# Performance work log

Measured on AMD Instinct MI355X. Metric: run time of the kernel, lower is better.

The kernel has to match this reference:

```python
import jax, jax.numpy as jnp
import numpy as np
import math

B, S, D, H = 2, 4096, 768, 12
HD = D // H            # 64
BLK = 32               # MRA block size (hard-coded in the module)
NBR = S // BLK         # 128 blocks per row
NUM_BLOCK = 1024       # selected score blocks per (batch*head)
APPROX_MODE = "full"
FIRST_N = 0            # initial_prior_first_n_blocks
DIAG_N = 3             # initial_prior_diagonal_n_blocks
MB = B * H


def setup_inputs() -> dict:
    key = jax.random.key(0)
    ks = jax.random.split(key, 4)
    scale = 0.02
    return {
        "X": jax.random.normal(ks[0], (B, S, D), jnp.float32),
        "mask": jnp.ones((B, S), jnp.float32),
        "Wq": scale * jax.random.normal(ks[1], (D, D), jnp.float32),
        "bq": jnp.zeros((D,), jnp.float32),
        "Wk": scale * jax.random.normal(ks[2], (D, D), jnp.float32),
        "bk": jnp.zeros((D,), jnp.float32),
        "Wv": scale * jax.random.normal(ks[3], (D, D), jnp.float32),
        "bv": jnp.zeros((D,), jnp.float32),
    }


def _mra2_attention(Q, K, V, mask):
    # Q, K, V: [MB, S, HD]; mask: [MB, S] (float 0/1)
    inv_sqrt_d = 1.0 / math.sqrt(HD)
    Q = Q * mask[:, :, None]
    K = K * mask[:, :, None]
    V = V * mask[:, :, None]

    # ---- low-resolution (block-mean) logits ----
    token_count = mask.reshape(MB, NBR, BLK).sum(-1)                 # [MB, NBR]
    denom = token_count[:, :, None] + 1e-6
    Qh = Q.reshape(MB, NBR, BLK, HD).sum(2) / denom                  # [MB, NBR, HD]
    Kh = K.reshape(MB, NBR, BLK, HD).sum(2) / denom
    Vh = V.reshape(MB, NBR, BLK, HD).sum(2) / denom

    low_logit = jnp.einsum('bnd,bmd->bnm', Qh, Kh) * inv_sqrt_d      # [MB, NBR, NBR]
    row_max = low_logit.max(-1, keepdims=True)                        # [MB, NBR, 1] (before empty-pair masking)
    pair_empty = (token_count[:, None, :] * token_count[:, :, None]) < 0.5
    low_logit = low_logit - 1e4 * pair_empty.astype(low_logit.dtype)

    # ---- top-k block selection (no grad) ----
    prior = jax.lax.stop_gradient(low_logit - row_max)
    if DIAG_N > 0:
        off = DIAG_N // 2
        i = jnp.arange(NBR)
        band = (jnp.abs(i[:, None] - i[None, :]) <= off).astype(prior.dtype)
        prior = prior + band[None] * 5e3
    if FIRST_N > 0:
        prior = prior.at[:, :FIRST_N, :].add(5e3)
        prior = prior.at[:, :, :FIRST_N].add(5e3)
    top_vals, indices = jax.lax.top_k(prior.reshape(MB, -1), NUM_BLOCK)  # row-major flat idx = q_blk*NBR + k_blk
    threshold = top_vals.min(-1)
    selected_mask = (prior >= threshold[:, None, None]).astype(jnp.float32)  # 1 for selected low-res blocks

    rblk = indices // NBR   # query block index, [MB, NUM_BLOCK]
    cblk = indices % NBR    # key block index
    bidx = jnp.arange(MB)[:, None]

    Qb = Q.reshape(MB, NBR, BLK, HD)
    Kb = K.reshape(MB, NBR, BLK, HD)
    Vb = V.reshape(MB, NBR, BLK, HD)
    kmask = mask.reshape(MB, NBR, BLK)[bidx, cblk]                   # [MB, NB, 32k]

    Qg = Qb[bidx, rblk]                                              # [MB, NB, 32, HD]
    Kg = Kb[bidx, cblk]
    Vg = Vb[bidx, cblk]

    # ---- high-resolution sparse block logits ----
    logit = jnp.einsum('bnqd,bnkd->bnqk', Qg, Kg) * inv_sqrt_d       # [MB, NB, 32q, 32k]

    seg = (jnp.arange(MB)[:, None] * NBR + rblk).reshape(-1)         # segment id per block -> query row block
    blk_qmax = logit.max(-1).reshape(MB * NUM_BLOCK, BLK)            # per-query-token max within block
    max_rows = jax.ops.segment_max(blk_qmax, seg, num_segments=MB * NBR)
    max_rows = jnp.maximum(max_rows, -1e6).reshape(MB, NBR, BLK)     # guard rows w/o selected blocks
    max_vals = max_rows.reshape(MB, S)                               # per-token sparse row max
    max_scatter = max_rows[bidx, rblk]                               # [MB, NB, 32q]

    logit = logit - max_scatter[:, :, :, None]
    logit = logit - 1e4 * (1.0 - kmask[:, :, None, :])
    attn = jnp.exp(logit)

    blk_out = jnp.einsum('bnqk,bnkd->bnqd', attn, Vg)                # [MB, NB, 32, HD]
    high_out = jax.ops.segment_sum(
        blk_out.reshape(MB * NUM_BLOCK, BLK, HD), seg, num_segments=MB * NBR
    ).reshape(MB, S, HD)
    high_norm = jax.ops.segment_sum(
        attn.sum(-1).reshape(MB * NUM_BLOCK, BLK), seg, num_segments=MB * NBR
    ).reshape(MB, S)

    if APPROX_MODE == "full":
        # low-res attention over NON-selected blocks, weighted by token counts
        low_attn = jnp.exp(low_logit - row_max - 1e4 * selected_mask) * token_count[:, None, :]
        low_out = jnp.einsum('bnm,bmd->bnd', low_attn, Vh)           # [MB, NBR, HD]
        low_out = jnp.repeat(low_out[:, :, None, :], BLK, axis=2).reshape(MB, S, HD)
        low_norm = jnp.repeat(low_attn.sum(-1)[:, :, None], BLK, axis=2).reshape(MB, S)

        log_corr = jnp.repeat(row_max, BLK, axis=2).reshape(MB, S) - max_vals
        log_corr = log_corr * mask
        low_corr = jnp.exp(jnp.minimum(log_corr, 0.0))
        high_corr = jnp.exp(-jnp.maximum(log_corr, 0.0))

        out = (high_out * high_corr[:, :, None] + low_out * low_corr[:, :, None]) / (
            (high_norm * high_corr + low_norm * low_corr + 1e-6)[:, :, None]
        )
    else:  # "sparse"
        out = high_out / (high_norm[:, :, None] + 1e-6)
    return out


def reference(X, mask, Wq, bq, Wk, bk, Wv, bv):
    def proj(W, b):
        y = jnp.einsum('bsd,ed->bse', X, W) + b                       # nn.Linear: x @ W.T + b
        return y.reshape(B, S, H, HD).transpose(0, 2, 1, 3).reshape(MB, S, HD)

    Q, K, V = proj(Wq, bq), proj(Wk, bk), proj(Wv, bv)
    m = jnp.broadcast_to(mask[:, None, :], (B, H, S)).reshape(MB, S)
    out = _mra2_attention(Q, K, V, m)
    return out.reshape(B, H, S, HD).transpose(0, 2, 1, 3).reshape(B, S, D)
```

## Files before the change

### kernel.cpp

```cpp
#include <hip/hip_runtime.h>

typedef __bf16 bf16;
typedef float f32x4 __attribute__((ext_vector_type(4)));
typedef bf16 bf16x8 __attribute__((ext_vector_type(8)));
typedef bf16 bf16x4 __attribute__((ext_vector_type(4)));
typedef unsigned int uint;
typedef unsigned short ushort;


__device__ __forceinline__ void llds16(const bf16* g, bf16* l) {
    __builtin_amdgcn_global_load_lds((const __attribute__((address_space(1))) uint*)g,
                                     (__attribute__((address_space(3))) uint*)l, 16, 0, 0);
}

__device__ __forceinline__ uint sortable(float f) {
    uint u = __float_as_uint(f);
    return u ^ (uint)(((int)u >> 31) | 0x80000000);
}

__global__ __launch_bounds__(256)
void k_prep(const float* __restrict__ X, const float* __restrict__ mask,
            bf16* __restrict__ Xb, float* __restrict__ Xh, float* __restrict__ tc) {
    const int row = blockIdx.x;
    const int b = row >> 7, nbr = row & 127;
    const int g = blockIdx.y;
    const int t = threadIdx.x;
    const int c = t & 63;
    const int tq = t >> 6;
    const int c4 = g * 64 + c;
    const size_t base = (size_t)(b * 4096 + nbr * 32) * 768;
    const float4* xp = (const float4*)(X + base) + c4;
    bf16x4* xbp = (bf16x4*)(Xb + base) + c4;
    const float* mp = mask + b * 4096 + nbr * 32;
    __shared__ float4 red[4][64];
    __shared__ float tcr[4];
    float4 s = {0.f, 0.f, 0.f, 0.f};
    float tcs = 0.f;
#pragma unroll
    for (int j = 0; j < 8; ++j) {
        const int tok = tq * 8 + j;
        float4 v = xp[(size_t)tok * 192];
        float m = mp[tok];
        s.x += v.x * m; s.y += v.y * m; s.z += v.z * m; s.w += v.w * m;
        tcs += m;
        bf16x4 o = {(bf16)v.x, (bf16)v.y, (bf16)v.z, (bf16)v.w};
        xbp[(size_t)tok * 192] = o;
    }
    red[tq][c] = s;
    if (c == 0) tcr[tq] = tcs;
    __syncthreads();
    if (tq == 0) {
        float4 a = red[0][c], b2 = red[1][c], c2 = red[2][c], d2 = red[3][c];
        float4 o = {a.x + b2.x + c2.x + d2.x, a.y + b2.y + c2.y + d2.y,
                    a.z + b2.z + c2.z + d2.z, a.w + b2.w + c2.w + d2.w};
        ((float4*)(Xh + (size_t)row * 768))[c4] = o;
        if (c == 0 && g == 0) tc[row] = tcr[0] + tcr[1] + tcr[2] + tcr[3];
    }
}

__global__ void k_convW(const float* __restrict__ Wq, const float* __restrict__ Wk,
                        const float* __restrict__ Wv, bf16* __restrict__ Wb) {
    int i = blockIdx.x * 256 + threadIdx.x;
    if (i >= 442368) return;
    int n = (i << 2) / 768;
    int k = (i << 2) % 768;
    const float* W = n < 768 ? Wq : (n < 1536 ? Wk : Wv);
    int nn = n - (n < 768 ? 0 : (n < 1536 ? 768 : 1536));
    float4 f = *(const float4*)(W + (size_t)nn * 768 + k);
    bf16x4 o = {(bf16)f.x, (bf16)f.y, (bf16)f.z, (bf16)f.w};
    ((bf16x4*)Wb)[i] = o;
}

__global__ __launch_bounds__(256, 4)
void k_gemm_qkv(const bf16* __restrict__ Xb, const bf16* __restrict__ Wb,
                const float* __restrict__ bq, const float* __restrict__ bk,
                const float* __restrict__ bv, const float* __restrict__ mask,
                bf16* __restrict__ Qb, bf16* __restrict__ Kb, bf16* __restrict__ Vt) {
    __shared__ bf16 smem[17408];
    bf16* As = smem;
    bf16* Bs = smem + 8192;
    const int tid = threadIdx.x;
    const int wave = tid >> 6, lane = tid & 63;
    const int quad = lane >> 4, l16 = lane & 15;
    const int wr = wave >> 1, wc = wave & 1;
    const int m0 = blockIdx.x * 128, n0 = blockIdx.y * 128;
    const int srow = lane >> 3;
    const int sgcol = (((lane & 7) ^ (srow & 7)) << 3);

    f32x4 acc[4][4] = {};

    for (int k0 = 0; k0 < 768; k0 += 64) {
        __syncthreads();
#pragma unroll
        for (int it = 0; it < 4; ++it) {
            int R = wave * 32 + it * 8;
            llds16(Xb + (size_t)(m0 + R + srow) * 768 + k0 + sgcol, &As[R * 64]);
            llds16(Wb + (size_t)(n0 + R + srow) * 768 + k0 + sgcol, &Bs[R * 64]);
        }
        __syncthreads();
#pragma unroll
        for (int ks = 0; ks < 2; ++ks) {
            const int pg = ((ks * 4 + quad) ^ (l16 & 7)) << 3;
            bf16x8 a[4], b[4];
#pragma unroll
            for (int i = 0; i < 4; ++i)
                a[i] = *(const bf16x8*)&As[(wr * 64 + i * 16 + l16) * 64 + pg];
#pragma unroll
            for (int i = 0; i < 4; ++i)
                b[i] = *(const bf16x8*)&Bs[(wc * 64 + i * 16 + l16) * 64 + pg];
#pragma unroll
            for (int i = 0; i < 4; ++i)
#pragma unroll
                for (int j = 0; j < 4; ++j)
                    acc[i][j] = __builtin_amdgcn_mfma_f32_16x16x32_bf16(a[i], b[j], acc[i][j], 0, 0, 0);
        }
    }

    const int which = n0 / 768;
    const float* bias = which == 0 ? bq : (which == 1 ? bk : bv);

    __syncthreads();
#pragma unroll
    for (int i = 0; i < 4; ++i) {
        const int rloc0 = wr * 64 + i * 16 + quad * 4;
#pragma unroll
        for (int j = 0; j < 4; ++j) {
            const int cloc = wc * 64 + j * 16 + l16;
            const int hcol = n0 - which * 768 + cloc;
            const float bv_ = bias[hcol];
#pragma unroll
            for (int r = 0; r < 4; ++r) {
                const int rloc = rloc0 + r;
                const int mm = m0 + rloc;
                const int bidx = mm >> 12, s = mm & 4095;
                const float y = (acc[i][j][r] + bv_) * mask[(bidx << 12) + s];
                if (which == 2) smem[cloc * 136 + rloc] = (bf16)y;
                else            smem[rloc * 136 + cloc] = (bf16)y;
            }
        }
    }
    __syncthreads();
    if (which < 2) {
        bf16* dst = which == 0 ? Qb : Kb;
#pragma unroll
        for (int it = 0; it < 8; ++it) {
            const int gidx = it * 256 + tid;
            const int sr = gidx >> 4, chunk = gidx & 15;
            const int mm = m0 + sr;
            const int bidx = mm >> 12, s = mm & 4095;
            const int hcol = n0 - which * 768 + chunk * 8;
            const int h = hcol >> 6, d0 = hcol & 63;
            bf16x8 v = *(const bf16x8*)&smem[sr * 136 + chunk * 8];
            *(bf16x8*)(dst + ((((size_t)(bidx * 12 + h)) << 12) + s) * 64 + d0) = v;
        }
    } else {
#pragma unroll
        for (int it = 0; it < 8; ++it) {
            const int gidx = it * 256 + tid;
            const int drow = gidx >> 4, chunk = gidx & 15;
            const int s0 = chunk * 8;
            const int mm = m0 + s0;
            const int bidx = mm >> 12, s = mm & 4095;
            const int hcol = n0 - 1536 + drow;
            const int h = hcol >> 6, dd = hcol & 63;
            bf16x8 v = *(const bf16x8*)&smem[drow * 136 + s0];
            *(bf16x8*)(Vt + ((((size_t)(bidx * 12 + h)) * 128 + (s >> 5)) * 64 + dd) * 32 + (s & 31)) = v;
        }
    }
}

__global__ __launch_bounds__(256)
void k_lowres_p(const float* __restrict__ Xh,
                const float* __restrict__ Wq, const float* __restrict__ Wk,
                const float* __restrict__ Wv, float* __restrict__ partial) {
    const int nb = blockIdx.x;
    const int rowbase = blockIdx.y * 128;
    const int bz = blockIdx.z;
    const int kb = bz * 112;
    const int klen = (bz == 6) ? 96 : 112;
    const int t = threadIdx.x;

    __shared__ float As[16 * 132];
    __shared__ float Bs[16 * 132];

    const int which = nb / 6;
    const float* Wsel = which == 0 ? Wq : (which == 1 ? Wk : Wv);
    const float* Wbase = Wsel + (size_t)((nb % 6) * 128) * 768;

    const int sr = t >> 2;
    const int skq = t & 3;
    const int tr = t >> 4, tc2 = t & 15;
    const int r0 = tr * 8, c0 = tc2 * 8;

    float acc[8][8] = {};
    float4 va[2], vb[2];
    const int stages = klen >> 4;

#pragma unroll
    for (int i = 0; i < 2; ++i) {
        va[i] = *(const float4*)(Xh + (size_t)(rowbase + sr + 64 * i) * 768 + kb + skq * 4);
        vb[i] = *(const float4*)(Wbase + (size_t)(sr + 64 * i) * 768 + kb + skq * 4);
    }

    for (int s = 0; s < stages; ++s) {
        __syncthreads();
#pragma unroll
        for (int i = 0; i < 2; ++i) {
            const int r = sr + 64 * i;
            As[(skq * 4 + 0) * 132 + r] = va[i].x;
            As[(skq * 4 + 1) * 132 + r] = va[i].y;
            As[(skq * 4 + 2) * 132 + r] = va[i].z;
            As[(skq * 4 + 3) * 132 + r] = va[i].w;
            Bs[(skq * 4 + 0) * 132 + r] = vb[i].x;
            Bs[(skq * 4 + 1) * 132 + r] = vb[i].y;
            Bs[(skq * 4 + 2) * 132 + r] = vb[i].z;
            Bs[(skq * 4 + 3) * 132 + r] = vb[i].w;
        }
        if (s + 1 < stages) {
            const int kc = kb + (s + 1) * 16;
#pragma unroll
            for (int i = 0; i < 2; ++i) {
                va[i] = *(const float4*)(Xh + (size_t)(rowbase + sr + 64 * i) * 768 + kc + skq * 4);
                vb[i] = *(const float4*)(Wbase + (size_t)(sr + 64 * i) * 768 + kc + skq * 4);
            }
        }
        __syncthreads();
#pragma unroll
        for (int k = 0; k < 16; ++k) {
            float4 a0 = *(const float4*)&As[k * 132 + r0];
            float4 a1 = *(const float4*)&As[k * 132 + r0 + 4];
            float4 b0 = *(const float4*)&Bs[k * 132 + c0];
            float4 b1 = *(const float4*)&Bs[k * 132 + c0 + 4];
            float av[8] = {a0.x, a0.y, a0.z, a0.w, a1.x, a1.y, a1.z, a1.w};
            float bv[8] = {b0.x, b0.y, b0.z, b0.w, b1.x, b1.y, b1.z, b1.w};
#pragma unroll
            for (int i = 0; i < 8; ++i)
#pragma unroll
                for (int j = 0; j < 8; ++j)
                    acc[i][j] += av[i] * bv[j];
        }
    }

    float* pp = partial + (size_t)bz * 589824 + (size_t)(rowbase + r0) * 2304 + nb * 128 + c0;
#pragma unroll
    for (int i = 0; i < 8; ++i) {
        float4 s0 = {acc[i][0], acc[i][1], acc[i][2], acc[i][3]};
        float4 s1 = {acc[i][4], acc[i][5], acc[i][6], acc[i][7]};
        *(float4*)(pp + (size_t)i * 2304) = s0;
        *(float4*)(pp + (size_t)i * 2304 + 4) = s1;
    }
}

__global__ __launch_bounds__(256)
void k_lowfin(const float* __restrict__ partial, const float* __restrict__ tc,
              const float* __restrict__ bq, const float* __restrict__ bk,
              const float* __restrict__ bv,
              float* __restrict__ Qh, float* __restrict__ Kh, float* __restrict__ Vh) {
    const int gx = blockIdx.x;
    const int row = blockIdx.y;
    const int t = threadIdx.x;
    const int gcol = gx * 256 + t;
    float s = 0.f;
#pragma unroll
    for (int ch = 0; ch < 7; ++ch)
        s += partial[(size_t)ch * 589824 + (size_t)row * 2304 + gcol];
    const int which = gx / 3;
    const int wcol = (gx % 3) * 256 + t;
    const float* bias = which == 0 ? bq : (which == 1 ? bk : bv);
    const float tcv = tc[row];
    const float val = (s + tcv * bias[wcol]) / (tcv + 1e-6f);
    const int b = row >> 7, nbr = row & 127;
    const int h = wcol >> 6, d = wcol & 63;
    float* dst = which == 0 ? Qh : (which == 1 ? Kh : Vh);
    dst[(((size_t)(b * 12 + h)) * 128 + nbr) * 64 + d] = val;
}

__global__ __launch_bounds__(256)
void k_lowlogit(const float* __restrict__ Qh, const float* __restrict__ Kh,
                float* __restrict__ prior, float* __restrict__ rowmax) {
    int mb = blockIdx.x, rc = blockIdx.y;
    int tid = threadIdx.x;
    __shared__ float Ksh[64 * 132];
    __shared__ float Qsh[16 * 64];
    for (int idx = tid; idx < 128 * 64; idx += 256) {
        int c = idx >> 6, k = idx & 63;
        Ksh[k * 132 + c] = Kh[((size_t)mb * 128 + c) * 64 + k];
    }
    for (int idx = tid; idx < 16 * 64; idx += 256) {
        int r = idx >> 6, k = idx & 63;
        Qsh[idx] = Qh[((size_t)mb * 128 + rc * 16 + r) * 64 + k];
    }
    __syncthreads();
    int rloc = tid >> 4, cg = tid & 15;
    float acc[8] = {};
    for (int k = 0; k < 64; ++k) {
        float qv = Qsh[rloc * 64 + k];
        const float* kr = &Ksh[k * 132 + cg * 8];
#pragma unroll
        for (int j = 0; j < 8; ++j) acc[j] += qv * kr[j];
    }
    float pm = -3.4e38f;
#pragma unroll
    for (int j = 0; j < 8; ++j) { acc[j] *= 0.125f; pm = fmaxf(pm, acc[j]); }
#pragma unroll
    for (int d = 1; d < 16; d <<= 1) pm = fmaxf(pm, __shfl_xor(pm, d, 64));
    int r = rc * 16 + rloc;
    if (cg == 0) rowmax[mb * 128 + r] = pm;
    float* dst = prior + ((size_t)mb * 128 + r) * 128 + cg * 8;
#pragma unroll
    for (int j = 0; j < 8; ++j) dst[j] = acc[j] - pm;
}

__global__ __launch_bounds__(1024)
void k_select(const float* __restrict__ prior, unsigned char* __restrict__ selmask,
              unsigned short* __restrict__ lists, int* __restrict__ counts,
              ushort* __restrict__ qorder) {
    const int mb = blockIdx.x, tid = threadIdx.x;
    const int ln = tid & 63;
    __shared__ int lc[16 * 3];
    __shared__ int cnt[128];
    if (tid < 48) lc[tid] = 0;
    if (tid < 128) cnt[tid] = 0;

    const int r = tid >> 3;
    const int cbase = (tid & 7) << 4;
    uint key[16];
    const float4* P4 = (const float4*)(prior + (size_t)mb * 16384) + (tid << 2);
#pragma unroll
    for (int j4 = 0; j4 < 4; ++j4) {
        float4 v = P4[j4];
        float vv[4] = {v.x, v.y, v.z, v.w};
#pragma unroll
        for (int e = 0; e < 4; ++e) {
            int c = cbase + (j4 << 2) + e;
            float f = vv[e] + ((r - c <= 1 && c - r <= 1) ? 5e3f : 0.f);
            key[(j4 << 2) + e] = sortable(f);
        }
    }
    __syncthreads();

    uint pfx = 0u;
    int k = 1024;
#pragma unroll
    for (int lvl = 0; lvl < 16; ++lvl) {
        const int sh = 30 - 2 * lvl;
        const uint maskA = (lvl == 0) ? 0u : (0xFFFFFFFFu << (sh + 2));
        int c3 = 0, c2 = 0, c1 = 0;
#pragma unroll
        for (int j = 0; j < 16; ++j) {
            uint x = key[j];
            bool m = ((x ^ pfx) & maskA) == 0u;
            uint f = (x >> sh) & 3u;
            c3 += (m && f == 3u);
            c2 += (m && f == 2u);
            c1 += (m && f == 1u);
        }
#pragma unroll
        for (int d = 1; d < 64; d <<= 1) {
            c3 += __shfl_xor(c3, d, 64);
            c2 += __shfl_xor(c2, d, 64);
            c1 += __shfl_xor(c1, d, 64);
        }
        if (ln == 0) {
            atomicAdd(&lc[lvl * 3 + 0], c3);
            atomicAdd(&lc[lvl * 3 + 1], c2);
            atomicAdd(&lc[lvl * 3 + 2], c1);
        }
        __syncthreads();
        const int C3 = lc[lvl * 3 + 0], C2 = lc[lvl * 3 + 1], C1 = lc[lvl * 3 + 2];
        uint choose;
        if (C3 >= k)                { choose = 3u; }
        else if (C3 + C2 >= k)      { choose = 2u; k -= C3; }
        else if (C3 + C2 + C1 >= k) { choose = 1u; k -= C3 + C2; }
        else                        { choose = 0u; k -= C3 + C2 + C1; }
        pfx |= choose << sh;
    }
    const uint T = pfx;

    uint packed[4] = {0u, 0u, 0u, 0u};
#pragma unroll
    for (int j = 0; j < 16; ++j) {
        if (key[j] >= T) {
            packed[j >> 2] |= 1u << ((j & 3) << 3);
            int pos = atomicAdd(&cnt[r], 1);
            lists[((size_t)mb * 128 + r) * 128 + pos] = (unsigned short)(cbase + j);
        }
    }
    uint4 pk;
    pk.x = packed[0]; pk.y = packed[1]; pk.z = packed[2]; pk.w = packed[3];
    *(uint4*)(selmask + (size_t)mb * 16384 + (size_t)tid * 16) = pk;
    __syncthreads();
    if (tid < 128) {
        const int myc = cnt[tid];
        counts[mb * 128 + tid] = myc;
        int rank = 0;
        for (int j = 0; j < 128; ++j) {
            int cj = cnt[j];
            rank += (cj > myc) || (cj == myc && j < tid);
        }
        qorder[mb * 128 + rank] = (ushort)tid;
    }
}

__global__ __launch_bounds__(64)
void k_lowout(const float* __restrict__ prior, const unsigned char* __restrict__ selmask,
              const float* __restrict__ tc, const float* __restrict__ Vh,
              float* __restrict__ low_out, float* __restrict__ low_norm) {
    const int q = blockIdx.x & 127, mb = blockIdx.x >> 7;
    const int d = threadIdx.x;
    const float* pn = prior + ((size_t)mb * 128 + q) * 128;
    const uint4* smv = (const uint4*)(selmask + ((size_t)mb * 128 + q) * 128);
    uint sm32[32];
#pragma unroll
    for (int w = 0; w < 8; ++w) {
        uint4 u = smv[w];
        sm32[w * 4 + 0] = u.x; sm32[w * 4 + 1] = u.y;
        sm32[w * 4 + 2] = u.z; sm32[w * 4 + 3] = u.w;
    }
    const float* tcb = tc + (mb / 12) * 128;
    const float* Vb = Vh + (size_t)mb * 128 * 64;
    float acc = 0.f, nrm = 0.f;
#pragma unroll 4
    for (int c = 0; c < 128; ++c) {
        if (!((sm32[c >> 2] >> ((c & 3) << 3)) & 1u)) {
            float w = __expf(pn[c]) * tcb[c];
            acc += w * Vb[c * 64 + d];
            nrm += w;
        }
    }
    low_out[((size_t)mb * 128 + q) * 64 + d] = acc;
    if (d == 0) low_norm[mb * 128 + q] = nrm;
}

__global__ __launch_bounds__(64)
void k_high(const bf16* __restrict__ Qb, const bf16* __restrict__ Kb,
            const bf16* __restrict__ Vt, const int* __restrict__ counts,
            const unsigned short* __restrict__ lists, const ushort* __restrict__ qorder,
            const float* __restrict__ rowmax, const float* __restrict__ low_out,
            const float* __restrict__ low_norm, const float* __restrict__ mask,
            float* __restrict__ out) {
    const int bid = blockIdx.x;
    const int work = ((bid & 7) * 384) + (bid >> 3);
    const int mb = work >> 7;
    const int q = qorder[mb * 128 + (work & 127)];
    const int lane = threadIdx.x, quad = lane >> 4, l16 = lane & 15;
    __shared__ bf16 Pa[32 * 40];
    __shared__ bf16 Pbs[32 * 40];

    const bf16* Qbase = Qb + ((size_t)mb * 4096 + q * 32) * 64;
    bf16x8 qf[2][2];
#pragma unroll
    for (int mt = 0; mt < 2; ++mt)
#pragma unroll
        for (int ks = 0; ks < 2; ++ks)
            qf[mt][ks] = *(const bf16x8*)(Qbase + (mt * 16 + l16) * 64 + ks * 32 + quad * 8);

    bf16x8 ones;
#pragma unroll
    for (int j = 0; j < 8; ++j) ones[j] = (bf16)1.0f;

    float mxl[2][4];
    f32x4 o[2][4] = {};
    f32x4 lac[2] = {};
#pragma unroll
    for (int mt = 0; mt < 2; ++mt)
#pragma unroll
        for (int r = 0; r < 4; ++r) mxl[mt][r] = -3.4e38f;

    int cntv = counts[mb * 128 + q];
    if (cntv > 128) cntv = 128;
    if (cntv < 1) cntv = 1;
    const uint* lst32 = (const uint*)(lists + ((size_t)mb * 128 + q) * 128);

    const bf16* KB = Kb + (size_t)mb * 4096 * 64;
    const bf16* VB = Vt + (size_t)mb * 128 * 2048;

    int koff[2][2], voff[4];
#pragma unroll
    for (int nt = 0; nt < 2; ++nt)
#pragma unroll
        for (int ks = 0; ks < 2; ++ks) koff[nt][ks] = (nt * 16 + l16) * 64 + ks * 32 + quad * 8;
#pragma unroll
    for (int nd = 0; nd < 4; ++nd) voff[nd] = (nd * 16 + l16) * 32 + quad * 8;

    bf16x8 kA[2][2], vA[4], kB[2][2], vB[4];
    {
        const uint pr = lst32[0];
        const int cA = __builtin_amdgcn_readfirstlane((int)(pr & 0xffffu));
        const bf16* kp = KB + (size_t)cA * 2048;
        const bf16* vp = VB + (size_t)cA * 2048;
#pragma unroll
        for (int nt = 0; nt < 2; ++nt)
#pragma unroll
            for (int ks = 0; ks < 2; ++ks) kA[nt][ks] = *(const bf16x8*)(kp + koff[nt][ks]);
#pragma unroll
        for (int nd = 0; nd < 4; ++nd) vA[nd] = *(const bf16x8*)(vp + voff[nd]);
        if (cntv > 1) {
            const int cB = __builtin_amdgcn_readfirstlane((int)(pr >> 16));
            const bf16* kp2 = KB + (size_t)cB * 2048;
            const bf16* vp2 = VB + (size_t)cB * 2048;
#pragma unroll
            for (int nt = 0; nt < 2; ++nt)
#pragma unroll
                for (int ks = 0; ks < 2; ++ks) kB[nt][ks] = *(const bf16x8*)(kp2 + koff[nt][ks]);
#pragma unroll
            for (int nd = 0; nd < 4; ++nd) vB[nd] = *(const bf16x8*)(vp2 + voff[nd]);
        }
    }

    for (int i = 0; i < cntv; i += 2) {
        const bool hasB = (i + 1 < cntv);
        const bool hasAn = (i + 2 < cntv);
        const bool hasBn = (i + 3 < cntv);
        int cAn = 0, cBn = 0;
        if (hasAn) {
            const uint prn = lst32[(i >> 1) + 1];
            cAn = __builtin_amdgcn_readfirstlane((int)(prn & 0xffffu));
            cBn = __builtin_amdgcn_readfirstlane((int)(prn >> 16));
        }

        {
            f32x4 sf[2][2] = {};
            __builtin_amdgcn_s_setprio(1);
#pragma unroll
            for (int mt = 0; mt < 2; ++mt)
#pragma unroll
                for (int nt = 0; nt < 2; ++nt) {
                    sf[mt][nt] = __builtin_amdgcn_mfma_f32_16x16x32_bf16(qf[mt][0], kA[nt][0], sf[mt][nt], 0, 0, 0);
                    sf[mt][nt] = __builtin_amdgcn_mfma_f32_16x16x32_bf16(qf[mt][1], kA[nt][1], sf[mt][nt], 0, 0, 0);
                }
            __builtin_amdgcn_s_setprio(0);
#pragma unroll
            for (int mt = 0; mt < 2; ++mt)
#pragma unroll
                for (int r = 0; r < 4; ++r) {
                    mxl[mt][r] = fmaxf(mxl[mt][r], fmaxf(sf[mt][0][r], sf[mt][1][r]));
                    float e0, e1;
                    asm("v_exp_f32 %0, %1" : "=v"(e0) : "v"(sf[mt][0][r] * 0.18033688011112042f));
                    asm("v_exp_f32 %0, %1" : "=v"(e1) : "v"(sf[mt][1][r] * 0.18033688011112042f));
                    Pa[(mt * 16 + quad * 4 + r) * 40 + l16] = (bf16)e0;
                    Pa[(mt * 16 + quad * 4 + r) * 40 + 16 + l16] = (bf16)e1;
                }
        }
        if (hasB) {
            f32x4 sf[2][2] = {};
            __builtin_amdgcn_s_setprio(1);
#pragma unroll
            for (int mt = 0; mt < 2; ++mt)
#pragma unroll
                for (int nt = 0; nt < 2; ++nt) {
                    sf[mt][nt] = __builtin_amdgcn_mfma_f32_16x16x32_bf16(qf[mt][0], kB[nt][0], sf[mt][nt], 0, 0, 0);
                    sf[mt][nt] = __builtin_amdgcn_mfma_f32_16x16x32_bf16(qf[mt][1], kB[nt][1], sf[mt][nt], 0, 0, 0);
                }
            __builtin_amdgcn_s_setprio(0);
#pragma unroll
            for (int mt = 0; mt < 2; ++mt)
#pragma unroll
                for (int r = 0; r < 4; ++r) {
                    mxl[mt][r] = fmaxf(mxl[mt][r], fmaxf(sf[mt][0][r], sf[mt][1][r]));
                    float e0, e1;
                    asm("v_exp_f32 %0, %1" : "=v"(e0) : "v"(sf[mt][0][r] * 0.18033688011112042f));
                    asm("v_exp_f32 %0, %1" : "=v"(e1) : "v"(sf[mt][1][r] * 0.18033688011112042f));
                    Pbs[(mt * 16 + quad * 4 + r) * 40 + l16] = (bf16)e0;
                    Pbs[(mt * 16 + quad * 4 + r) * 40 + 16 + l16] = (bf16)e1;
                }
        }

        if (hasAn) {
            const bf16* kp = KB + (size_t)cAn * 2048;
#pragma unroll
            for (int nt = 0; nt < 2; ++nt)
#pragma unroll
                for (int ks = 0; ks < 2; ++ks) kA[nt][ks] = *(const bf16x8*)(kp + koff[nt][ks]);
        }
        if (hasBn) {
            const bf16* kp = KB + (size_t)cBn * 2048;
#pragma unroll
            for (int nt = 0; nt < 2; ++nt)
#pragma unroll
                for (int ks = 0; ks < 2; ++ks) kB[nt][ks] = *(const bf16x8*)(kp + koff[nt][ks]);
        }

        asm volatile("s_waitcnt lgkmcnt(0)" ::: "memory");
        bf16x8 pa[2], pb[2];
#pragma unroll
        for (int mt = 0; mt < 2; ++mt)
            pa[mt] = *(const bf16x8*)&Pa[(mt * 16 + l16) * 40 + quad * 8];
        if (hasB) {
#pragma unroll
            for (int mt = 0; mt < 2; ++mt)
                pb[mt] = *(const bf16x8*)&Pbs[(mt * 16 + l16) * 40 + quad * 8];
        }
        __builtin_amdgcn_s_setprio(1);
#pragma unroll
        for (int mt = 0; mt < 2; ++mt) {
#pragma unroll
            for (int nd = 0; nd < 4; ++nd)
                o[mt][nd] = __builtin_amdgcn_mfma_f32_16x16x32_bf16(pa[mt], vA[nd], o[mt][nd], 0, 0, 0);
            lac[mt] = __builtin_amdgcn_mfma_f32_16x16x32_bf16(pa[mt], ones, lac[mt], 0, 0, 0);
        }
        if (hasB) {
#pragma unroll
            for (int mt = 0; mt < 2; ++mt) {
#pragma unroll
                for (int nd = 0; nd < 4; ++nd)
                    o[mt][nd] = __builtin_amdgcn_mfma_f32_16x16x32_bf16(pb[mt], vB[nd], o[mt][nd], 0, 0, 0);
                lac[mt] = __builtin_amdgcn_mfma_f32_16x16x32_bf16(pb[mt], ones, lac[mt], 0, 0, 0);
            }
        }
        __builtin_amdgcn_s_setprio(0);

        if (hasAn) {
            const bf16* vp = VB + (size_t)cAn * 2048;
#pragma unroll
            for (int nd = 0; nd < 4; ++nd) vA[nd] = *(const bf16x8*)(vp + voff[nd]);
        }
        if (hasBn) {
            const bf16* vp = VB + (size_t)cBn * 2048;
#pragma unroll
            for (int nd = 0; nd < 4; ++nd) vB[nd] = *(const bf16x8*)(vp + voff[nd]);
        }
    }

#pragma unroll
    for (int d = 1; d < 16; d <<= 1)
#pragma unroll
        for (int mt = 0; mt < 2; ++mt)
#pragma unroll
            for (int r = 0; r < 4; ++r)
                mxl[mt][r] = fmaxf(mxl[mt][r], __shfl_xor(mxl[mt][r], d, 64));

    const int b = mb / 12, h = mb - b * 12;
    const float rm = rowmax[mb * 128 + q];
    const float ln = low_norm[mb * 128 + q];
    const float* LO = low_out + ((size_t)mb * 128 + q) * 64;
#pragma unroll
    for (int mt = 0; mt < 2; ++mt)
#pragma unroll
        for (int r = 0; r < 4; ++r) {
            const int s = q * 32 + mt * 16 + quad * 4 + r;
            const float mv = fmaxf(mxl[mt][r] * 0.125f, -1e6f);
            const float hn = lac[mt][r];
            const float mk = mask[(b << 12) + s];
            const float lcr = (rm - mv) * mk;
            const float lcf = __expf(fminf(lcr, 0.f));
            const float hcf = __expf(-mv - fmaxf(lcr, 0.f));
            const float den = 1.0f / (hn * hcf + ln * lcf + 1e-6f);
            float* op = out + ((size_t)(b * 4096 + s)) * 768 + h * 64;
#pragma unroll
            for (int nd = 0; nd < 4; ++nd) {
                const int d = nd * 16 + l16;
                op[d] = (o[mt][nd][r] * hcf + LO[d] * lcf) * den;
            }
        }
}

extern "C" void kernel_launch(void* const* d_in, const int* in_sizes, int n_in,
                              void* d_out, int out_size, void* d_ws, size_t ws_size,
                              hipStream_t stream) {
    (void)in_sizes; (void)n_in; (void)out_size; (void)ws_size;
    const float* X    = (const float*)d_in[0];
    const float* mask = (const float*)d_in[1];
    const float* Wq   = (const float*)d_in[2];
    const float* bq   = (const float*)d_in[3];
    const float* Wk   = (const float*)d_in[4];
    const float* bk   = (const float*)d_in[5];
    const float* Wv   = (const float*)d_in[6];
    const float* bv   = (const float*)d_in[7];
    float* out = (float*)d_out;

    char* ws = (char*)d_ws;
    size_t off = 0;
    auto alloc = [&](size_t bytes) -> void* {
        off = (off + 255) & ~(size_t)255;
        void* p = ws + off;
        off += bytes;
        return p;
    };
    bf16* Xb  = (bf16*)alloc((size_t)8192 * 768 * 2);
    bf16* Wb  = (bf16*)alloc((size_t)2304 * 768 * 2);
    bf16* Qb  = (bf16*)alloc((size_t)24 * 4096 * 64 * 2);
    bf16* Kb  = (bf16*)alloc((size_t)24 * 4096 * 64 * 2);
    bf16* Vt  = (bf16*)alloc((size_t)24 * 4096 * 64 * 2);
    float* Xh = (float*)alloc((size_t)256 * 768 * 4);
    float* tc = (float*)alloc(256 * 4);
    float* Qh = (float*)alloc((size_t)24 * 128 * 64 * 4);
    float* Kh = (float*)alloc((size_t)24 * 128 * 64 * 4);
    float* Vh = (float*)alloc((size_t)24 * 128 * 64 * 4);
    float* prior = (float*)alloc((size_t)24 * 16384 * 4);
    float* rowmax = (float*)alloc(24 * 128 * 4);
    unsigned char* selmask = (unsigned char*)alloc((size_t)24 * 16384);
    unsigned short* lists = (unsigned short*)alloc((size_t)24 * 128 * 128 * 2);
    int* counts = (int*)alloc(24 * 128 * 4);
    ushort* qorder = (ushort*)alloc(24 * 128 * 2);
    float* low_out   = (float*)alloc((size_t)24 * 128 * 64 * 4);
    float* low_norm  = (float*)alloc(24 * 128 * 4);
    float* partial   = (float*)alloc((size_t)7 * 589824 * 4);

    k_prep<<<dim3(256, 3), 256, 0, stream>>>(X, mask, Xb, Xh, tc);
    k_convW<<<1728, 256, 0, stream>>>(Wq, Wk, Wv, Wb);
    k_gemm_qkv<<<dim3(64, 18), 256, 0, stream>>>(Xb, Wb, bq, bk, bv, mask, Qb, Kb, Vt);
    k_lowres_p<<<dim3(18, 2, 7), 256, 0, stream>>>(Xh, Wq, Wk, Wv, partial);
    k_lowfin<<<dim3(9, 256), 256, 0, stream>>>(partial, tc, bq, bk, bv, Qh, Kh, Vh);
    k_lowlogit<<<dim3(24, 8), 256, 0, stream>>>(Qh, Kh, prior, rowmax);
    k_select<<<24, 1024, 0, stream>>>(prior, selmask, lists, counts, qorder);
    k_lowout<<<3072, 64, 0, stream>>>(prior, selmask, tc, Vh, low_out, low_norm);
    k_high<<<3072, 64, 0, stream>>>(Qb, Kb, Vt, counts, lists, qorder, rowmax, low_out,
                                    low_norm, mask, out);
}
```

Before: 268.3 us.

## Fuse weight conversion into prep and low-res output into high-res kernel

Merges the weight bf16 conversion kernel into the prep kernel as extra blocks, and computes the low-resolution attention output per query block inside k_high, after the first K/V prefetch is issued, instead of in a separate k_lowout kernel. This removes two kernel launches and the low_out/low_norm round-trip through global memory, and lets the low-res loop overlap with outstanding K/V loads. In exchange, k_high does more scalar work per block and holds more registers, and the low-res value is redistributed across lanes with shuffles during the output store.

Result: faster. 260.4 us (-2.9%).

```diff
diff --git a/kernel.cpp b/kernel.cpp
--- a/kernel.cpp
+++ b/kernel.cpp
@@ -20,11 +20,27 @@
 
 __global__ __launch_bounds__(256)
 void k_prep(const float* __restrict__ X, const float* __restrict__ mask,
-            bf16* __restrict__ Xb, float* __restrict__ Xh, float* __restrict__ tc) {
-    const int row = blockIdx.x;
+            const float* __restrict__ Wq, const float* __restrict__ Wk,
+            const float* __restrict__ Wv,
+            bf16* __restrict__ Xb, float* __restrict__ Xh, float* __restrict__ tc,
+            bf16* __restrict__ Wb) {
+    const int p = blockIdx.x;
+    const int t = threadIdx.x;
+    if (p >= 768) {
+        int i = (p - 768) * 256 + t;
+        if (i >= 442368) return;
+        int n = (i << 2) / 768;
+        int k = (i << 2) % 768;
+        const float* W = n < 768 ? Wq : (n < 1536 ? Wk : Wv);
+        int nn = n - (n < 768 ? 0 : (n < 1536 ? 768 : 1536));
+        float4 f = *(const float4*)(W + (size_t)nn * 768 + k);
+        bf16x4 o = {(bf16)f.x, (bf16)f.y, (bf16)f.z, (bf16)f.w};
+        ((bf16x4*)Wb)[i] = o;
+        return;
+    }
+    const int row = p % 256;
+    const int g = p / 256;
     const int b = row >> 7, nbr = row & 127;
-    const int g = blockIdx.y;
-    const int t = threadIdx.x;
     const int c = t & 63;
     const int tq = t >> 6;
     const int c4 = g * 64 + c;
@@ -56,19 +72,6 @@
         ((float4*)(Xh + (size_t)row * 768))[c4] = o;
         if (c == 0 && g == 0) tc[row] = tcr[0] + tcr[1] + tcr[2] + tcr[3];
     }
-}
-
-__global__ void k_convW(const float* __restrict__ Wq, const float* __restrict__ Wk,
-                        const float* __restrict__ Wv, bf16* __restrict__ Wb) {
-    int i = blockIdx.x * 256 + threadIdx.x;
-    if (i >= 442368) return;
-    int n = (i << 2) / 768;
-    int k = (i << 2) % 768;
-    const float* W = n < 768 ? Wq : (n < 1536 ? Wk : Wv);
-    int nn = n - (n < 768 ? 0 : (n < 1536 ? 768 : 1536));
-    float4 f = *(const float4*)(W + (size_t)nn * 768 + k);
-    bf16x4 o = {(bf16)f.x, (bf16)f.y, (bf16)f.z, (bf16)f.w};
-    ((bf16x4*)Wb)[i] = o;
 }
 
 __global__ __launch_bounds__(256, 4)
@@ -403,41 +406,12 @@
 }
 
 __global__ __launch_bounds__(64)
-void k_lowout(const float* __restrict__ prior, const unsigned char* __restrict__ selmask,
-              const float* __restrict__ tc, const float* __restrict__ Vh,
-              float* __restrict__ low_out, float* __restrict__ low_norm) {
-    const int q = blockIdx.x & 127, mb = blockIdx.x >> 7;
-    const int d = threadIdx.x;
-    const float* pn = prior + ((size_t)mb * 128 + q) * 128;
-    const uint4* smv = (const uint4*)(selmask + ((size_t)mb * 128 + q) * 128);
-    uint sm32[32];
-#pragma unroll
-    for (int w = 0; w < 8; ++w) {
-        uint4 u = smv[w];
-        sm32[w * 4 + 0] = u.x; sm32[w * 4 + 1] = u.y;
-        sm32[w * 4 + 2] = u.z; sm32[w * 4 + 3] = u.w;
-    }
-    const float* tcb = tc + (mb / 12) * 128;
-    const float* Vb = Vh + (size_t)mb * 128 * 64;
-    float acc = 0.f, nrm = 0.f;
-#pragma unroll 4
-    for (int c = 0; c < 128; ++c) {
-        if (!((sm32[c >> 2] >> ((c & 3) << 3)) & 1u)) {
-            float w = __expf(pn[c]) * tcb[c];
-            acc += w * Vb[c * 64 + d];
-            nrm += w;
-        }
-    }
-    low_out[((size_t)mb * 128 + q) * 64 + d] = acc;
-    if (d == 0) low_norm[mb * 128 + q] = nrm;
-}
-
-__global__ __launch_bounds__(64)
 void k_high(const bf16* __restrict__ Qb, const bf16* __restrict__ Kb,
             const bf16* __restrict__ Vt, const int* __restrict__ counts,
             const unsigned short* __restrict__ lists, const ushort* __restrict__ qorder,
-            const float* __restrict__ rowmax, const float* __restrict__ low_out,
-            const float* __restrict__ low_norm, const float* __restrict__ mask,
+            const float* __restrict__ rowmax, const float* __restrict__ prior,
+            const unsigned char* __restrict__ selmask, const float* __restrict__ tc,
+            const float* __restrict__ Vh, const float* __restrict__ mask,
             float* __restrict__ out) {
     const int bid = blockIdx.x;
     const int work = ((bid & 7) * 384) + (bid >> 3);
@@ -505,6 +479,22 @@
                 for (int ks = 0; ks < 2; ++ks) kB[nt][ks] = *(const bf16x8*)(kp2 + koff[nt][ks]);
 #pragma unroll
             for (int nd = 0; nd < 4; ++nd) vB[nd] = *(const bf16x8*)(vp2 + voff[nd]);
+        }
+    }
+
+    float lo = 0.f, ln = 0.f;
+    {
+        const float* pn = prior + ((size_t)mb * 128 + q) * 128;
+        const uint* sel32 = (const uint*)(selmask + ((size_t)mb * 128 + q) * 128);
+        const float* tcb = tc + (mb / 12) * 128;
+        const float* Vb = Vh + (size_t)mb * 128 * 64;
+#pragma unroll 4
+        for (int c = 0; c < 128; ++c) {
+            if (!((sel32[c >> 2] >> ((c & 3) << 3)) & 1u)) {
+                float w = __expf(pn[c]) * tcb[c];
+                lo += w * Vb[c * 64 + lane];
+                ln += w;
+            }
         }
     }
 
@@ -632,8 +622,6 @@
 
     const int b = mb / 12, h = mb - b * 12;
     const float rm = rowmax[mb * 128 + q];
-    const float ln = low_norm[mb * 128 + q];
-    const float* LO = low_out + ((size_t)mb * 128 + q) * 64;
 #pragma unroll
     for (int mt = 0; mt < 2; ++mt)
 #pragma unroll
@@ -650,7 +638,8 @@
 #pragma unroll
             for (int nd = 0; nd < 4; ++nd) {
                 const int d = nd * 16 + l16;
-                op[d] = (o[mt][nd][r] * hcf + LO[d] * lcf) * den;
+                const float LOd = __shfl(lo, d, 64);
+                op[d] = (o[mt][nd][r] * hcf + LOd * lcf) * den;
             }
         }
 }
@@ -693,18 +682,14 @@
     unsigned short* lists = (unsigned short*)alloc((size_t)24 * 128 * 128 * 2);
     int* counts = (int*)alloc(24 * 128 * 4);
     ushort* qorder = (ushort*)alloc(24 * 128 * 2);
-    float* low_out   = (float*)alloc((size_t)24 * 128 * 64 * 4);
-    float* low_norm  = (float*)alloc(24 * 128 * 4);
     float* partial   = (float*)alloc((size_t)7 * 589824 * 4);
 
-    k_prep<<<dim3(256, 3), 256, 0, stream>>>(X, mask, Xb, Xh, tc);
-    k_convW<<<1728, 256, 0, stream>>>(Wq, Wk, Wv, Wb);
+    k_prep<<<2496, 256, 0, stream>>>(X, mask, Wq, Wk, Wv, Xb, Xh, tc, Wb);
     k_gemm_qkv<<<dim3(64, 18), 256, 0, stream>>>(Xb, Wb, bq, bk, bv, mask, Qb, Kb, Vt);
     k_lowres_p<<<dim3(18, 2, 7), 256, 0, stream>>>(Xh, Wq, Wk, Wv, partial);
     k_lowfin<<<dim3(9, 256), 256, 0, stream>>>(partial, tc, bq, bk, bv, Qh, Kh, Vh);
     k_lowlogit<<<dim3(24, 8), 256, 0, stream>>>(Qh, Kh, prior, rowmax);
     k_select<<<24, 1024, 0, stream>>>(prior, selmask, lists, counts, qorder);
-    k_lowout<<<3072, 64, 0, stream>>>(prior, selmask, tc, Vh, low_out, low_norm);
-    k_high<<<3072, 64, 0, stream>>>(Qb, Kb, Vt, counts, lists, qorder, rowmax, low_out,
-                                    low_norm, mask, out);
-}
+    k_high<<<3072, 64, 0, stream>>>(Qb, Kb, Vt, counts, lists, qorder, rowmax, prior,
+                                    selmask, tc, Vh, mask, out);
+}
```
